# Optimization experiments

Measured on AMD Instinct MI355X. Metric: run time of the kernel, lower is better.

The kernel has to match this reference:

```python
import jax, jax.numpy as jnp
import numpy as np

NL = 4      # num_hidden_layers
NH = 12     # self-attn heads
CH = 4      # cross-attn heads (hardcoded in module)
S = 4       # speakers per dialog
EPS = 1e-5

def layernorm(x, g, b):
    m = x.mean(-1, keepdims=True)
    v = jnp.mean((x - m) ** 2, axis=-1, keepdims=True)
    return (x - m) * jax.lax.rsqrt(v + EPS) * g + b

def self_mha(x, in_w, in_b, out_w, out_b):
    # x: [B,T,L,H] self-attention over L (the per-turn token axis)
    B, T, L, H = x.shape
    dh = H // NH
    qkv = x @ in_w + in_b                       # [B,T,L,3H]
    q, k, v = jnp.split(qkv, 3, axis=-1)
    q = q.reshape(B, T, L, NH, dh); k = k.reshape(B, T, L, NH, dh); v = v.reshape(B, T, L, NH, dh)
    s = jnp.einsum('btqhd,btkhd->bthqk', q, k) / np.sqrt(dh).astype(x.dtype)
    a = jax.nn.softmax(s, axis=-1)
    o = jnp.einsum('bthqk,btkhd->btqhd', a, v).reshape(B, T, L, H)
    return o @ out_w + out_b

def forward(input_ids, attention_mask, speaker_ids, tok_emb, pos_emb, turn_emb,
            mha_in_w, mha_in_b, mha_out_w, mha_out_b,
            ffn_w1, ffn_b1, ffn_w2, ffn_b2,
            ln1_g, ln1_b, ln2_g, ln2_b,
            gate_w, gate_b, sn_g, sn_b,
            ca_in_w, ca_in_b, ca_out_w, ca_out_b):
    B, T, L = input_ids.shape
    H = tok_emb.shape[1]
    X = tok_emb[input_ids] + pos_emb[jnp.arange(L)][None, None] + turn_emb[jnp.arange(T)][None, :, None]
    mask = attention_mask[..., None].astype(X.dtype)            # [B,T,L,1]
    onehot = (speaker_ids[..., None] == jnp.arange(S)).astype(X.dtype)  # [B,T,S]
    counts = onehot.sum(1)                                      # [B,S]
    M = jnp.zeros((B, S, H), X.dtype)                           # speaker memory
    for l in range(NL):
        m_t = jnp.einsum('bts,bsh->bth', onehot, M)             # gather memory per turn
        h = (X + m_t[:, :, None, :]) * mask                     # mask applied by zeroing inputs (as in source)
        h = self_mha(h, mha_in_w[l], mha_in_b[l], mha_out_w[l], mha_out_b[l])
        h = layernorm(h + X, ln1_g[l], ln1_b[l])
        ffn = jax.nn.gelu(h @ ffn_w1[l] + ffn_b1[l], approximate=False) @ ffn_w2[l] + ffn_b2[l]
        h = layernorm(h + ffn, ln2_g[l], ln2_b[l])
        X = h
        tc = h.mean(2)                                          # token_context [B,T,H]
        # cross-attention: each turn's context queries its dialog's speaker memory
        wq, wk, wv = jnp.split(ca_in_w[l], 3, axis=-1)
        bq, bk, bv = jnp.split(ca_in_b[l], 3)
        dh = H // CH
        q = (tc @ wq + bq).reshape(B, T, CH, dh)
        k = (M @ wk + bk).reshape(B, S, CH, dh)
        v = (M @ wv + bv).reshape(B, S, CH, dh)
        s = jnp.einsum('bthd,bshd->bhts', q, k) / np.sqrt(dh).astype(X.dtype)
        a = jax.nn.softmax(s, axis=-1)
        cc = jnp.einsum('bhts,bshd->bthd', a, v).reshape(B, T, H) @ ca_out_w[l] + ca_out_b[l]
        fused = jnp.concatenate([tc, m_t, cc], axis=-1)         # [B,T,3H]
        upd = layernorm(fused @ gate_w[l] + gate_b[l] + m_t, sn_g[l], sn_b[l])
        # scatter: per-speaker mean over that speaker's turns; untouched speakers keep old memory
        sums = jnp.einsum('bts,bth->bsh', onehot, upd)
        mean = sums / jnp.maximum(counts, 1.0)[..., None]
        M = jnp.where((counts > 0)[..., None], mean, M)
    return X, M

def setup_inputs() -> dict:
    key = jax.random.key(0)
    ks = iter(jax.random.split(key, 32))
    B, T, L, H, F, V, P = 8, 64, 64, 768, 3072, 30522, 512
    n = lambda shape: jax.random.normal(next(ks), shape, jnp.float32) * 0.02
    return {
        'input_ids': jax.random.randint(next(ks), (B, T, L), 0, V, jnp.int32),
        'attention_mask': jax.random.randint(next(ks), (B, T, L), 0, 2, jnp.int32),
        'speaker_ids': jax.random.randint(next(ks), (B, T), 0, S, jnp.int32),
        'tok_emb': n((V, H)), 'pos_emb': n((P, H)), 'turn_emb': n((P, H)),
        'mha_in_w': n((NL, H, 3 * H)), 'mha_in_b': jnp.zeros((NL, 3 * H)),
        'mha_out_w': n((NL, H, H)), 'mha_out_b': jnp.zeros((NL, H)),
        'ffn_w1': n((NL, H, F)), 'ffn_b1': jnp.zeros((NL, F)),
        'ffn_w2': n((NL, F, H)), 'ffn_b2': jnp.zeros((NL, H)),
        'ln1_g': jnp.ones((NL, H)), 'ln1_b': jnp.zeros((NL, H)),
        'ln2_g': jnp.ones((NL, H)), 'ln2_b': jnp.zeros((NL, H)),
        'gate_w': n((NL, 3 * H, H)), 'gate_b': jnp.zeros((NL, H)),
        'sn_g': jnp.ones((NL, H)), 'sn_b': jnp.zeros((NL, H)),
        'ca_in_w': n((NL, H, 3 * H)), 'ca_in_b': jnp.zeros((NL, 3 * H)),
        'ca_out_w': n((NL, H, H)), 'ca_out_b': jnp.zeros((NL, H)),
    }

def reference(input_ids, attention_mask, speaker_ids, tok_emb, pos_emb, turn_emb,
              mha_in_w, mha_in_b, mha_out_w, mha_out_b,
              ffn_w1, ffn_b1, ffn_w2, ffn_b2,
              ln1_g, ln1_b, ln2_g, ln2_b,
              gate_w, gate_b, sn_g, sn_b,
              ca_in_w, ca_in_b, ca_out_w, ca_out_b):
    return forward(input_ids, attention_mask, speaker_ids, tok_emb, pos_emb, turn_emb,
                   mha_in_w, mha_in_b, mha_out_w, mha_out_b,
                   ffn_w1, ffn_b1, ffn_w2, ffn_b2,
                   ln1_g, ln1_b, ln2_g, ln2_b,
                   gate_w, gate_b, sn_g, sn_b,
                   ca_in_w, ca_in_b, ca_out_w, ca_out_b)
```

## Files before the change

kernel.cpp:

```cpp
#include <hip/hip_runtime.h>

using u16 = unsigned short;
using u32 = unsigned int;

#define DI __device__ __forceinline__

typedef __bf16 bf16x8 __attribute__((ext_vector_type(8)));
typedef float  f32x4  __attribute__((ext_vector_type(4)));

DI float b2f(u16 u){ u32 x = ((u32)u) << 16; float f; __builtin_memcpy(&f, &x, 4); return f; }
DI u16 f2b(float f){ __bf16 h = (__bf16)f; u16 r; __builtin_memcpy(&r, &h, 2); return r; }
DI float gelu_fast(float v){
    float u = v * (0.7978845608f + 0.0356774081f * v * v);
    float e = __expf(2.0f * u);
    float t = 1.0f - 2.0f / (e + 1.0f);
    return 0.5f * v * (1.0f + t);
}

#define GLOAD16(g, l) __builtin_amdgcn_global_load_lds( \
    (const __attribute__((address_space(1))) void*)(g), \
    (__attribute__((address_space(3))) void*)(l), 16, 0, 0)

template<int EPI>
__global__ __launch_bounds__(256)
void gemm_bt(const u16* __restrict__ A, const u16* __restrict__ Bt,
             const float* __restrict__ bias, void* __restrict__ Cout,
             int M, int N, int K)
{
    __shared__ u16 lA[128 * 32];
    __shared__ u16 lB[128 * 32];
    const int tid  = threadIdx.x;
    const int lane = tid & 63;
    const int w    = tid >> 6;
    const int wm   = w >> 1, wn = w & 1;

    const int nx = gridDim.x;
    const int nb = nx * gridDim.y;
    int bid = blockIdx.y * nx + blockIdx.x;
    if ((nb & 7) == 0) bid = ((bid & 7) * (nb >> 3)) + (bid >> 3);
    const int m0 = (bid / nx) * 128;
    const int n0 = (bid % nx) * 128;

    f32x4 acc[4][4] = {};

    const int srow = tid >> 2;
    const int scol = (tid & 3) * 8;
    int ar0 = m0 + srow;      if (ar0 > M - 1) ar0 = M - 1;
    int ar1 = m0 + 64 + srow; if (ar1 > M - 1) ar1 = M - 1;
    const u16* gA0 = A  + (size_t)ar0 * K + scol;
    const u16* gA1 = A  + (size_t)ar1 * K + scol;
    const u16* gB0 = Bt + (size_t)(n0 + srow) * K + scol;
    const u16* gB1 = Bt + (size_t)(n0 + 64 + srow) * K + scol;
    u16* dA = &lA[tid * 8];
    u16* dB = &lB[tid * 8];

    const int la = lane & 15, lg = lane >> 4;
    for (int k0 = 0; k0 < K; k0 += 32) {
        GLOAD16(gA0 + k0, dA);
        GLOAD16(gA1 + k0, dA + 2048);
        GLOAD16(gB0 + k0, dB);
        GLOAD16(gB1 + k0, dB + 2048);
        __syncthreads();
        bf16x8 af[4], bfr[4];
        #pragma unroll
        for (int i = 0; i < 4; i++)
            af[i] = *(const bf16x8*)&lA[(wm * 64 + i * 16 + la) * 32 + lg * 8];
        #pragma unroll
        for (int j = 0; j < 4; j++)
            bfr[j] = *(const bf16x8*)&lB[(wn * 64 + j * 16 + la) * 32 + lg * 8];
        #pragma unroll
        for (int i = 0; i < 4; i++)
            #pragma unroll
            for (int j = 0; j < 4; j++)
                acc[i][j] = __builtin_amdgcn_mfma_f32_16x16x32_bf16(af[i], bfr[j], acc[i][j], 0, 0, 0);
        __syncthreads();
    }

    #pragma unroll
    for (int i = 0; i < 4; i++) {
        const int rowb = m0 + wm * 64 + i * 16 + lg * 4;
        #pragma unroll
        for (int j = 0; j < 4; j++) {
            const int col = n0 + wn * 64 + j * 16 + la;
            const float bv = bias[col];
            #pragma unroll
            for (int r = 0; r < 4; r++) {
                const int rr = rowb + r;
                if (rr < M) {
                    float v = acc[i][j][r] + bv;
                    if constexpr (EPI == 1) v = gelu_fast(v);
                    if constexpr (EPI == 2) ((float*)Cout)[(size_t)rr * N + col] = v;
                    else                    ((u16*)Cout)[(size_t)rr * N + col] = f2b(v);
                }
            }
        }
    }
}

__global__ __launch_bounds__(256)
void transp_conv(const float* __restrict__ in, u16* __restrict__ out, int K, int N)
{
    __shared__ float tile[32][33];
    const int l = blockIdx.z;
    const float* inp = in + (size_t)l * K * N;
    u16* op = out + (size_t)l * K * N;
    const int kb = blockIdx.y * 32, nb = blockIdx.x * 32;
    const int tx = threadIdx.x, ty = threadIdx.y;
    #pragma unroll
    for (int i = 0; i < 32; i += 8)
        tile[ty + i][tx] = inp[(size_t)(kb + ty + i) * N + nb + tx];
    __syncthreads();
    #pragma unroll
    for (int i = 0; i < 32; i += 8)
        op[(size_t)(nb + ty + i) * K + kb + tx] = f2b(tile[tx][ty + i]);
}

__global__ __launch_bounds__(192)
void embed_k(const int* __restrict__ ids, const float* __restrict__ te,
             const float* __restrict__ pe, const float* __restrict__ ue,
             u16* __restrict__ X)
{
    const int tok = blockIdx.x;
    const int l = tok & 63;
    const int t = (tok >> 6) & 63;
    const int id = ids[tok];
    const int c = threadIdx.x * 4;
    float4 a = *(const float4*)&te[(size_t)id * 768 + c];
    float4 p = *(const float4*)&pe[(size_t)l * 768 + c];
    float4 u = *(const float4*)&ue[(size_t)t * 768 + c];
    ushort4 o;
    o.x = f2b(a.x + p.x + u.x); o.y = f2b(a.y + p.y + u.y);
    o.z = f2b(a.z + p.z + u.z); o.w = f2b(a.w + p.w + u.w);
    *(ushort4*)&X[(size_t)tok * 768 + c] = o;
}

__global__ __launch_bounds__(256)
void gather_mt(const float* __restrict__ M, const int* __restrict__ sid,
               float* __restrict__ mt)
{
    const int bt = blockIdx.x, b = bt >> 6, tid = threadIdx.x;
    const float* src = M + ((size_t)b * 4 + sid[bt]) * 768;
    float* dst = mt + (size_t)bt * 768;
    dst[tid] = src[tid]; dst[tid + 256] = src[tid + 256]; dst[tid + 512] = src[tid + 512];
}

__global__ __launch_bounds__(192)
void prep_ain(const u16* __restrict__ X, const float* __restrict__ mt,
              const int* __restrict__ mask, u16* __restrict__ Ain)
{
    const int tok = blockIdx.x, bt = tok >> 6;
    const float mk = (float)mask[tok];
    const int c = threadIdx.x * 4;
    ushort4 xv = *(const ushort4*)&X[(size_t)tok * 768 + c];
    float4 mv = *(const float4*)&mt[(size_t)bt * 768 + c];
    ushort4 o;
    o.x = f2b((b2f(xv.x) + mv.x) * mk); o.y = f2b((b2f(xv.y) + mv.y) * mk);
    o.z = f2b((b2f(xv.z) + mv.z) * mk); o.w = f2b((b2f(xv.w) + mv.w) * mk);
    *(ushort4*)&Ain[(size_t)tok * 768 + c] = o;
}

__global__ __launch_bounds__(256)
void attn_self(const u16* __restrict__ QKV, u16* __restrict__ O)
{
    __shared__ u16 lQ[64 * 64], lK[64 * 64], lVt[64 * 64], lP[64 * 64];
    __shared__ float lS[64 * 68];
    const int bt = blockIdx.x / 12, h = blockIdx.x % 12;
    const int tid = threadIdx.x, lane = tid & 63, w = tid >> 6;
    const size_t base = (size_t)bt * 64 * 2304;

    #pragma unroll
    for (int it = 0; it < 2; ++it) {
        const int slot = it * 256 + tid;
        const int l = slot >> 3, dc = (slot & 7) * 8;
        const u16* qp = QKV + base + (size_t)l * 2304 + h * 64 + dc;
        *(uint4*)&lQ[l * 64 + dc] = *(const uint4*)qp;
        *(uint4*)&lK[l * 64 + dc] = *(const uint4*)(qp + 768);
        uint4 vv = *(const uint4*)(qp + 1536);
        u16 tmp[8]; *(uint4*)tmp = vv;
        #pragma unroll
        for (int j = 0; j < 8; j++) lVt[(dc + j) * 64 + l] = tmp[j];
    }
    __syncthreads();

    const int la = lane & 15, lg = lane >> 4;
    {
        f32x4 sa[4] = {};
        #pragma unroll
        for (int kh = 0; kh < 64; kh += 32) {
            bf16x8 aq = *(const bf16x8*)&lQ[(w * 16 + la) * 64 + kh + lg * 8];
            #pragma unroll
            for (int fn = 0; fn < 4; ++fn) {
                bf16x8 bk = *(const bf16x8*)&lK[(fn * 16 + la) * 64 + kh + lg * 8];
                sa[fn] = __builtin_amdgcn_mfma_f32_16x16x32_bf16(aq, bk, sa[fn], 0, 0, 0);
            }
        }
        #pragma unroll
        for (int fn = 0; fn < 4; ++fn)
            #pragma unroll
            for (int r = 0; r < 4; ++r)
                lS[(w * 16 + lg * 4 + r) * 68 + fn * 16 + la] = sa[fn][r] * 0.125f;
    }
    __syncthreads();

    {
        const int row = tid >> 2, q4 = tid & 3;
        float e[16]; float mx = -1e30f;
        #pragma unroll
        for (int j = 0; j < 16; j++) { e[j] = lS[row * 68 + q4 * 16 + j]; mx = fmaxf(mx, e[j]); }
        mx = fmaxf(mx, __shfl_xor(mx, 1)); mx = fmaxf(mx, __shfl_xor(mx, 2));
        float sm = 0.f;
        #pragma unroll
        for (int j = 0; j < 16; j++) { e[j] = __expf(e[j] - mx); sm += e[j]; }
        sm += __shfl_xor(sm, 1); sm += __shfl_xor(sm, 2);
        const float inv = 1.0f / sm;
        #pragma unroll
        for (int j = 0; j < 16; j++) lP[row * 64 + q4 * 16 + j] = f2b(e[j] * inv);
    }
    __syncthreads();

    {
        f32x4 oa[4] = {};
        #pragma unroll
        for (int kh = 0; kh < 64; kh += 32) {
            bf16x8 ap = *(const bf16x8*)&lP[(w * 16 + la) * 64 + kh + lg * 8];
            #pragma unroll
            for (int fn = 0; fn < 4; ++fn) {
                bf16x8 bv = *(const bf16x8*)&lVt[(fn * 16 + la) * 64 + kh + lg * 8];
                oa[fn] = __builtin_amdgcn_mfma_f32_16x16x32_bf16(ap, bv, oa[fn], 0, 0, 0);
            }
        }
        const size_t ob = (size_t)bt * 64 * 768 + h * 64;
        #pragma unroll
        for (int fn = 0; fn < 4; ++fn)
            #pragma unroll
            for (int r = 0; r < 4; ++r)
                O[ob + (size_t)(w * 16 + lg * 4 + r) * 768 + fn * 16 + la] = f2b(oa[fn][r]);
    }
}

DI float wave_red(float v) {
    #pragma unroll
    for (int o = 32; o > 0; o >>= 1) v += __shfl_xor(v, o);
    return v;
}

__global__ __launch_bounds__(256)
void ln_res(const u16* __restrict__ a, const u16* __restrict__ b,
            const float* __restrict__ g, const float* __restrict__ be,
            u16* __restrict__ out)
{
    __shared__ float red[8];
    const int tid = threadIdx.x;
    const size_t off = (size_t)blockIdx.x * 768;
    float x0 = b2f(a[off + tid])       + b2f(b[off + tid]);
    float x1 = b2f(a[off + tid + 256]) + b2f(b[off + tid + 256]);
    float x2 = b2f(a[off + tid + 512]) + b2f(b[off + tid + 512]);
    float s = wave_red(x0 + x1 + x2);
    float ss = wave_red(x0 * x0 + x1 * x1 + x2 * x2);
    if ((tid & 63) == 0) { red[tid >> 6] = s; red[4 + (tid >> 6)] = ss; }
    __syncthreads();
    s = red[0] + red[1] + red[2] + red[3];
    ss = red[4] + red[5] + red[6] + red[7];
    const float mean = s * (1.f / 768.f);
    const float var = fmaxf(ss * (1.f / 768.f) - mean * mean, 0.f);
    const float inv = rsqrtf(var + 1e-5f);
    out[off + tid]       = f2b((x0 - mean) * inv * g[tid]       + be[tid]);
    out[off + tid + 256] = f2b((x1 - mean) * inv * g[tid + 256] + be[tid + 256]);
    out[off + tid + 512] = f2b((x2 - mean) * inv * g[tid + 512] + be[tid + 512]);
}

__global__ __launch_bounds__(256)
void ln_upd(const float* __restrict__ a, const float* __restrict__ b,
            const float* __restrict__ g, const float* __restrict__ be,
            float* __restrict__ out)
{
    __shared__ float red[8];
    const int tid = threadIdx.x;
    const size_t off = (size_t)blockIdx.x * 768;
    float x0 = a[off + tid]       + b[off + tid];
    float x1 = a[off + tid + 256] + b[off + tid + 256];
    float x2 = a[off + tid + 512] + b[off + tid + 512];
    float s = wave_red(x0 + x1 + x2);
    float ss = wave_red(x0 * x0 + x1 * x1 + x2 * x2);
    if ((tid & 63) == 0) { red[tid >> 6] = s; red[4 + (tid >> 6)] = ss; }
    __syncthreads();
    s = red[0] + red[1] + red[2] + red[3];
    ss = red[4] + red[5] + red[6] + red[7];
    const float mean = s * (1.f / 768.f);
    const float var = fmaxf(ss * (1.f / 768.f) - mean * mean, 0.f);
    const float inv = rsqrtf(var + 1e-5f);
    out[off + tid]       = (x0 - mean) * inv * g[tid]       + be[tid];
    out[off + tid + 256] = (x1 - mean) * inv * g[tid + 256] + be[tid + 256];
    out[off + tid + 512] = (x2 - mean) * inv * g[tid + 512] + be[tid + 512];
}

__global__ __launch_bounds__(256)
void tc_mean(const u16* __restrict__ X, u16* __restrict__ tcb)
{
    const int bt = blockIdx.x, tid = threadIdx.x;
    float s0 = 0, s1 = 0, s2 = 0;
    for (int l = 0; l < 64; ++l) {
        const u16* r = X + ((size_t)bt * 64 + l) * 768;
        s0 += b2f(r[tid]); s1 += b2f(r[tid + 256]); s2 += b2f(r[tid + 512]);
    }
    tcb[(size_t)bt * 768 + tid]       = f2b(s0 * (1.f / 64.f));
    tcb[(size_t)bt * 768 + tid + 256] = f2b(s1 * (1.f / 64.f));
    tcb[(size_t)bt * 768 + tid + 512] = f2b(s2 * (1.f / 64.f));
}

__global__ __launch_bounds__(256)
void conv_bf16(const float* __restrict__ in, u16* __restrict__ out, int n)
{
    const int i = blockIdx.x * 256 + threadIdx.x;
    if (i < n) out[i] = f2b(in[i]);
}

__global__ __launch_bounds__(256)
void zero_f32(float* __restrict__ buf, int n)
{
    const int i = blockIdx.x * 256 + threadIdx.x;
    if (i < n) buf[i] = 0.f;
}

__global__ __launch_bounds__(256)
void cross_attn(const u16* __restrict__ qc, const u16* __restrict__ kvc,
                u16* __restrict__ cca)
{
    __shared__ float q[768], kk[4][768], vv[4][768], sraw[16], aw[16];
    const int bt = blockIdx.x, b = bt >> 6, tid = threadIdx.x;
    #pragma unroll
    for (int i = 0; i < 3; i++) q[tid + i * 256] = b2f(qc[(size_t)bt * 768 + tid + i * 256]);
    #pragma unroll
    for (int i = 0; i < 12; i++) {
        const int idx = i * 256 + tid;
        const int s = idx / 768, d = idx % 768;
        kk[s][d] = b2f(kvc[(size_t)(b * 4 + s) * 1536 + d]);
        vv[s][d] = b2f(kvc[(size_t)(b * 4 + s) * 1536 + 768 + d]);
    }
    __syncthreads();
    if (tid < 16) {
        const int hh = tid >> 2, s = tid & 3;
        float acc = 0.f;
        for (int d = 0; d < 192; ++d) acc += q[hh * 192 + d] * kk[s][hh * 192 + d];
        sraw[tid] = acc * 0.07216878364870323f;
    }
    __syncthreads();
    if (tid < 4) {
        float m = -1e30f;
        for (int s = 0; s < 4; s++) m = fmaxf(m, sraw[tid * 4 + s]);
        float ee[4], sm = 0.f;
        for (int s = 0; s < 4; s++) { ee[s] = __expf(sraw[tid * 4 + s] - m); sm += ee[s]; }
        for (int s = 0; s < 4; s++) aw[tid * 4 + s] = ee[s] / sm;
    }
    __syncthreads();
    #pragma unroll
    for (int i = 0; i < 3; i++) {
        const int j = tid + i * 256;
        const int hh = j / 192;
        float v = aw[hh * 4 + 0] * vv[0][j] + aw[hh * 4 + 1] * vv[1][j]
                + aw[hh * 4 + 2] * vv[2][j] + aw[hh * 4 + 3] * vv[3][j];
        cca[(size_t)bt * 768 + j] = f2b(v);
    }
}

__global__ __launch_bounds__(256)
void concat_fused(const u16* __restrict__ tcb, const float* __restrict__ mt,
                  const u16* __restrict__ ccp, u16* __restrict__ Fu)
{
    const int bt = blockIdx.x, tid = threadIdx.x;
    u16* o = Fu + (size_t)bt * 2304;
    #pragma unroll
    for (int i = 0; i < 3; i++) {
        const int j = tid + i * 256;
        o[j]        = tcb[(size_t)bt * 768 + j];
        o[768 + j]  = f2b(mt[(size_t)bt * 768 + j]);
        o[1536 + j] = ccp[(size_t)bt * 768 + j];
    }
}

__global__ __launch_bounds__(256)
void scatter_mem(const float* __restrict__ upd, const int* __restrict__ sid,
                 const float* __restrict__ counts, float* __restrict__ M)
{
    const int bs = blockIdx.x, b = bs >> 2, s = bs & 3, tid = threadIdx.x;
    const float c = counts[bs];
    #pragma unroll
    for (int i = 0; i < 3; i++) {
        const int j = tid + i * 256;
        float acc = 0.f;
        for (int t = 0; t < 64; ++t)
            if (sid[b * 64 + t] == s) acc += upd[((size_t)b * 64 + t) * 768 + j];
        if (c > 0.f) M[(size_t)bs * 768 + j] = acc / fmaxf(c, 1.f);
    }
}

__global__ void calc_counts(const int* __restrict__ sid, float* __restrict__ counts)
{
    const int tid = threadIdx.x;
    if (tid < 32) {
        const int b = tid >> 2, s = tid & 3;
        float c = 0.f;
        for (int t = 0; t < 64; ++t) c += (sid[b * 64 + t] == s) ? 1.f : 0.f;
        counts[tid] = c;
    }
}

__global__ __launch_bounds__(256)
void final_out(const u16* __restrict__ Xb, const float* __restrict__ M,
               float* __restrict__ out)
{
    const size_t i = (size_t)blockIdx.x * 256 + threadIdx.x;
    const size_t NX = 25165824ull;
    if (i < NX) out[i] = b2f(Xb[i]);
    else if (i < NX + 24576ull) out[i] = M[i - NX];
}

extern "C" void kernel_launch(void* const* d_in, const int* in_sizes, int n_in,
                              void* d_out, int out_size, void* d_ws, size_t ws_size,
                              hipStream_t stream)
{
    const int*   input_ids = (const int*)d_in[0];
    const int*   attn_mask = (const int*)d_in[1];
    const int*   sid       = (const int*)d_in[2];
    const float* tok_emb   = (const float*)d_in[3];
    const float* pos_emb   = (const float*)d_in[4];
    const float* turn_emb  = (const float*)d_in[5];
    const float* mha_in_w  = (const float*)d_in[6];
    const float* mha_in_b  = (const float*)d_in[7];
    const float* mha_out_w = (const float*)d_in[8];
    const float* mha_out_b = (const float*)d_in[9];
    const float* ffn_w1    = (const float*)d_in[10];
    const float* ffn_b1    = (const float*)d_in[11];
    const float* ffn_w2    = (const float*)d_in[12];
    const float* ffn_b2    = (const float*)d_in[13];
    const float* ln1_g     = (const float*)d_in[14];
    const float* ln1_b     = (const float*)d_in[15];
    const float* ln2_g     = (const float*)d_in[16];
    const float* ln2_b     = (const float*)d_in[17];
    const float* gate_w    = (const float*)d_in[18];
    const float* gate_b    = (const float*)d_in[19];
    const float* sn_g      = (const float*)d_in[20];
    const float* sn_b      = (const float*)d_in[21];
    const float* ca_in_w   = (const float*)d_in[22];
    const float* ca_in_b   = (const float*)d_in[23];
    const float* ca_out_w  = (const float*)d_in[24];
    const float* ca_out_b  = (const float*)d_in[25];
    (void)in_sizes; (void)n_in; (void)out_size;

    const size_t MB = 1ull << 20;
    int NCA, NCF; bool allW;
    if      (ws_size >= 460 * MB) { NCA = 2; NCF = 1; allW = true;  }
    else if (ws_size >= 255 * MB) { NCA = 2; NCF = 2; allW = false; }
    else                          { NCA = 4; NCF = 4; allW = false; }
    const int MRA = 32768 / NCA;
    const int MRF = 32768 / NCF;
    const size_t wl = allW ? 4 : 1;

    char* p = (char*)d_ws;
    auto alloc = [&](size_t n) { void* r = p; p += (n + 255) & ~(size_t)255; return r; };
    u16*   Xb    = (u16*)alloc(50331648);
    u16*   Hb    = (u16*)alloc(50331648);
    u16*   WqkvT = (u16*)alloc(wl * 3538944);
    u16*   WoT   = (u16*)alloc(wl * 1179648);
    u16*   W1T   = (u16*)alloc(wl * 4718592);
    u16*   W2T   = (u16*)alloc(wl * 4718592);
    u16*   WgT   = (u16*)alloc(wl * 3538944);
    u16*   WcaT  = (u16*)alloc(wl * 3538944);
    u16*   WcoT  = (u16*)alloc(wl * 1179648);
    float* mt    = (float*)alloc(1572864);
    u16*   tcb   = (u16*)alloc(786432);
    u16*   Mb    = (u16*)alloc(49152);
    u16*   qc    = (u16*)alloc(786432);
    u16*   kvc   = (u16*)alloc(98304);
    u16*   cca   = (u16*)alloc(786432);
    u16*   ccp   = (u16*)alloc(786432);
    u16*   Fu    = (u16*)alloc(2359296);
    float* gout  = (float*)alloc(1572864);
    float* upd   = (float*)alloc(1572864);
    float* cnts  = (float*)alloc(256);
    float* M     = (float*)alloc(98304);

    u16 *A, *QKVb, *Gb;
    if (NCF == 1) {
        A    = (u16*)alloc(50331648);
        Gb   = (u16*)alloc(201326592);
        QKVb = (u16*)d_out;
    } else if (NCF == 2) {
        A    = (u16*)alloc(50331648);
        QKVb = (u16*)alloc((size_t)MRA * 2304 * 2);
        Gb   = (u16*)d_out;
    } else {
        Gb   = (u16*)alloc((size_t)MRF * 3072 * 2);
        A    = (u16*)d_out;
        QKVb = (u16*)d_out + 25165824;
    }
    u16* Obuf = Gb;

    zero_f32<<<96, 256, 0, stream>>>(M, 24576);
    calc_counts<<<1, 64, 0, stream>>>(sid, cnts);
    embed_k<<<32768, 192, 0, stream>>>(input_ids, tok_emb, pos_emb, turn_emb, Xb);

    if (allW) {
        transp_conv<<<dim3(72, 24, 4), dim3(32, 8), 0, stream>>>(mha_in_w,  WqkvT, 768, 2304);
        transp_conv<<<dim3(24, 24, 4), dim3(32, 8), 0, stream>>>(mha_out_w, WoT,   768, 768);
        transp_conv<<<dim3(96, 24, 4), dim3(32, 8), 0, stream>>>(ffn_w1,    W1T,   768, 3072);
        transp_conv<<<dim3(24, 96, 4), dim3(32, 8), 0, stream>>>(ffn_w2,    W2T,  3072, 768);
        transp_conv<<<dim3(24, 72, 4), dim3(32, 8), 0, stream>>>(gate_w,    WgT,  2304, 768);
        transp_conv<<<dim3(72, 24, 4), dim3(32, 8), 0, stream>>>(ca_in_w,   WcaT,  768, 2304);
        transp_conv<<<dim3(24, 24, 4), dim3(32, 8), 0, stream>>>(ca_out_w,  WcoT,  768, 768);
    }

    for (int l = 0; l < 4; ++l) {
        if (!allW) {
            transp_conv<<<dim3(72, 24), dim3(32, 8), 0, stream>>>(mha_in_w  + (size_t)l * 768 * 2304, WqkvT, 768, 2304);
            transp_conv<<<dim3(24, 24), dim3(32, 8), 0, stream>>>(mha_out_w + (size_t)l * 768 * 768,  WoT,   768, 768);
            transp_conv<<<dim3(96, 24), dim3(32, 8), 0, stream>>>(ffn_w1    + (size_t)l * 768 * 3072, W1T,   768, 3072);
            transp_conv<<<dim3(24, 96), dim3(32, 8), 0, stream>>>(ffn_w2    + (size_t)l * 3072 * 768, W2T,  3072, 768);
            transp_conv<<<dim3(24, 72), dim3(32, 8), 0, stream>>>(gate_w    + (size_t)l * 2304 * 768, WgT,  2304, 768);
            transp_conv<<<dim3(72, 24), dim3(32, 8), 0, stream>>>(ca_in_w   + (size_t)l * 768 * 2304, WcaT,  768, 2304);
            transp_conv<<<dim3(24, 24), dim3(32, 8), 0, stream>>>(ca_out_w  + (size_t)l * 768 * 768,  WcoT,  768, 768);
        }
        const u16* Wqkv_l = WqkvT + (size_t)(allW ? l : 0) * 2304 * 768;
        const u16* Wo_l   = WoT   + (size_t)(allW ? l : 0) * 768 * 768;
        const u16* W1_l   = W1T   + (size_t)(allW ? l : 0) * 768 * 3072;
        const u16* W2_l   = W2T   + (size_t)(allW ? l : 0) * 3072 * 768;
        const u16* Wg_l   = WgT   + (size_t)(allW ? l : 0) * 2304 * 768;
        const u16* Wca_l  = WcaT  + (size_t)(allW ? l : 0) * 768 * 2304;
        const u16* Wco_l  = WcoT  + (size_t)(allW ? l : 0) * 768 * 768;

        gather_mt<<<512, 256, 0, stream>>>(M, sid, mt);
        prep_ain<<<32768, 192, 0, stream>>>(Xb, mt, attn_mask, A);

        for (int c = 0; c < NCA; ++c) {
            u16* Ac = A + (size_t)c * MRA * 768;
            gemm_bt<0><<<dim3(18, MRA / 128), 256, 0, stream>>>(Ac, Wqkv_l, mha_in_b + l * 2304, QKVb, MRA, 2304, 768);
            attn_self<<<(MRA / 64) * 12, 256, 0, stream>>>(QKVb, Obuf);
            gemm_bt<0><<<dim3(6, MRA / 128), 256, 0, stream>>>(Obuf, Wo_l, mha_out_b + l * 768, Ac, MRA, 768, 768);
        }
        ln_res<<<32768, 256, 0, stream>>>(A, Xb, ln1_g + l * 768, ln1_b + l * 768, Hb);

        for (int c = 0; c < NCF; ++c) {
            u16* Hc = Hb + (size_t)c * MRF * 768;
            u16* Ac = A  + (size_t)c * MRF * 768;
            gemm_bt<1><<<dim3(24, MRF / 128), 256, 0, stream>>>(Hc, W1_l, ffn_b1 + l * 3072, Gb, MRF, 3072, 768);
            gemm_bt<0><<<dim3(6, MRF / 128), 256, 0, stream>>>(Gb, W2_l, ffn_b2 + l * 768, Ac, MRF, 768, 3072);
        }
        ln_res<<<32768, 256, 0, stream>>>(A, Hb, ln2_g + l * 768, ln2_b + l * 768, Xb);

        tc_mean<<<512, 256, 0, stream>>>(Xb, tcb);
        conv_bf16<<<96, 256, 0, stream>>>(M, Mb, 24576);
        gemm_bt<0><<<dim3(6, 4), 256, 0, stream>>>(tcb, WcaT + (size_t)(allW ? l : 0) * 768 * 2304, ca_in_b + l * 2304, qc, 512, 768, 768);
        gemm_bt<0><<<dim3(12, 1), 256, 0, stream>>>(Mb, Wca_l + 768 * 768, ca_in_b + l * 2304 + 768, kvc, 32, 1536, 768);
        cross_attn<<<512, 256, 0, stream>>>(qc, kvc, cca);
        gemm_bt<0><<<dim3(6, 4), 256, 0, stream>>>(cca, Wco_l, ca_out_b + l * 768, ccp, 512, 768, 768);
        concat_fused<<<512, 256, 0, stream>>>(tcb, mt, ccp, Fu);
        gemm_bt<2><<<dim3(6, 4), 256, 0, stream>>>(Fu, Wg_l, gate_b + l * 768, gout, 512, 768, 2304);
        ln_upd<<<512, 256, 0, stream>>>(gout, mt, sn_g + l * 768, sn_b + l * 768, upd);
        scatter_mem<<<32, 256, 0, stream>>>(upd, sid, cnts, M);
    }

    final_out<<<98400, 256, 0, stream>>>(Xb, M, (float*)d_out);
}
```

Before: 4.352 ms.

## Double-buffer GEMM LDS tiles, swizzle LDS layouts in GEMM and attention

The GEMM kernel now keeps two LDS stages, so global-to-LDS loads for the next K tile are issued while MFMAs run on the current one, with one barrier per iteration instead of two. The GEMM and self-attention LDS layouts use XOR swizzles to reduce bank conflicts on fragment reads. The cross-attention query projection now reads the Wca_l pointer instead of WcaT. This doubles GEMM LDS use, which can lower occupancy, and the weight-pointer change may alter which weights are used.

```diff
diff --git a/kernel.cpp b/kernel.cpp
--- a/kernel.cpp
+++ b/kernel.cpp
@@ -21,14 +21,20 @@
     (const __attribute__((address_space(1))) void*)(g), \
     (__attribute__((address_space(3))) void*)(l), 16, 0, 0)
 
+#define HARD_BARRIER() do { \
+    asm volatile("s_waitcnt vmcnt(0)" ::: "memory"); \
+    __builtin_amdgcn_s_barrier(); \
+    asm volatile("" ::: "memory"); \
+} while (0)
+
 template<int EPI>
 __global__ __launch_bounds__(256)
 void gemm_bt(const u16* __restrict__ A, const u16* __restrict__ Bt,
              const float* __restrict__ bias, void* __restrict__ Cout,
              int M, int N, int K)
 {
-    __shared__ u16 lA[128 * 32];
-    __shared__ u16 lB[128 * 32];
+    __shared__ u16 lA[2][128 * 32];
+    __shared__ u16 lB[2][128 * 32];
     const int tid  = threadIdx.x;
     const int lane = tid & 63;
     const int w    = tid >> 6;
@@ -44,36 +50,49 @@
     f32x4 acc[4][4] = {};
 
     const int srow = tid >> 2;
-    const int scol = (tid & 3) * 8;
+    const int scol = (((tid & 3) ^ ((tid >> 3) & 3)) * 8);
     int ar0 = m0 + srow;      if (ar0 > M - 1) ar0 = M - 1;
     int ar1 = m0 + 64 + srow; if (ar1 > M - 1) ar1 = M - 1;
     const u16* gA0 = A  + (size_t)ar0 * K + scol;
     const u16* gA1 = A  + (size_t)ar1 * K + scol;
     const u16* gB0 = Bt + (size_t)(n0 + srow) * K + scol;
     const u16* gB1 = Bt + (size_t)(n0 + 64 + srow) * K + scol;
-    u16* dA = &lA[tid * 8];
-    u16* dB = &lB[tid * 8];
 
     const int la = lane & 15, lg = lane >> 4;
-    for (int k0 = 0; k0 < K; k0 += 32) {
-        GLOAD16(gA0 + k0, dA);
-        GLOAD16(gA1 + k0, dA + 2048);
-        GLOAD16(gB0 + k0, dB);
-        GLOAD16(gB1 + k0, dB + 2048);
-        __syncthreads();
+    const int cp = (lg ^ ((la >> 1) & 3)) * 8;
+
+    const int nt = K >> 5;
+
+    GLOAD16(gA0, &lA[0][tid * 8]);
+    GLOAD16(gA1, &lA[0][tid * 8 + 2048]);
+    GLOAD16(gB0, &lB[0][tid * 8]);
+    GLOAD16(gB1, &lB[0][tid * 8 + 2048]);
+    HARD_BARRIER();
+
+    int cur = 0;
+    for (int t = 0; t < nt; ++t) {
+        if (t + 1 < nt) {
+            const int k0 = (t + 1) << 5;
+            const int b = cur ^ 1;
+            GLOAD16(gA0 + k0, &lA[b][tid * 8]);
+            GLOAD16(gA1 + k0, &lA[b][tid * 8 + 2048]);
+            GLOAD16(gB0 + k0, &lB[b][tid * 8]);
+            GLOAD16(gB1 + k0, &lB[b][tid * 8 + 2048]);
+        }
         bf16x8 af[4], bfr[4];
         #pragma unroll
         for (int i = 0; i < 4; i++)
-            af[i] = *(const bf16x8*)&lA[(wm * 64 + i * 16 + la) * 32 + lg * 8];
+            af[i] = *(const bf16x8*)&lA[cur][(wm * 64 + i * 16 + la) * 32 + cp];
         #pragma unroll
         for (int j = 0; j < 4; j++)
-            bfr[j] = *(const bf16x8*)&lB[(wn * 64 + j * 16 + la) * 32 + lg * 8];
+            bfr[j] = *(const bf16x8*)&lB[cur][(wn * 64 + j * 16 + la) * 32 + cp];
         #pragma unroll
         for (int i = 0; i < 4; i++)
             #pragma unroll
             for (int j = 0; j < 4; j++)
                 acc[i][j] = __builtin_amdgcn_mfma_f32_16x16x32_bf16(af[i], bfr[j], acc[i][j], 0, 0, 0);
-        __syncthreads();
+        HARD_BARRIER();
+        cur ^= 1;
     }
 
     #pragma unroll
@@ -159,6 +178,8 @@
     *(ushort4*)&Ain[(size_t)tok * 768 + c] = o;
 }
 
+DI int swz(int row, int col) { return row * 64 + (((col >> 3) ^ (row & 7)) << 3) + (col & 7); }
+
 __global__ __launch_bounds__(256)
 void attn_self(const u16* __restrict__ QKV, u16* __restrict__ O)
 {
@@ -173,12 +194,12 @@
         const int slot = it * 256 + tid;
         const int l = slot >> 3, dc = (slot & 7) * 8;
         const u16* qp = QKV + base + (size_t)l * 2304 + h * 64 + dc;
-        *(uint4*)&lQ[l * 64 + dc] = *(const uint4*)qp;
-        *(uint4*)&lK[l * 64 + dc] = *(const uint4*)(qp + 768);
+        *(uint4*)&lQ[swz(l, dc)] = *(const uint4*)qp;
+        *(uint4*)&lK[swz(l, dc)] = *(const uint4*)(qp + 768);
         uint4 vv = *(const uint4*)(qp + 1536);
         u16 tmp[8]; *(uint4*)tmp = vv;
         #pragma unroll
-        for (int j = 0; j < 8; j++) lVt[(dc + j) * 64 + l] = tmp[j];
+        for (int j = 0; j < 8; j++) lVt[swz(dc + j, l)] = tmp[j];
     }
     __syncthreads();
 
@@ -187,10 +208,10 @@
         f32x4 sa[4] = {};
         #pragma unroll
         for (int kh = 0; kh < 64; kh += 32) {
-            bf16x8 aq = *(const bf16x8*)&lQ[(w * 16 + la) * 64 + kh + lg * 8];
+            bf16x8 aq = *(const bf16x8*)&lQ[swz(w * 16 + la, kh + lg * 8)];
             #pragma unroll
             for (int fn = 0; fn < 4; ++fn) {
-                bf16x8 bk = *(const bf16x8*)&lK[(fn * 16 + la) * 64 + kh + lg * 8];
+                bf16x8 bk = *(const bf16x8*)&lK[swz(fn * 16 + la, kh + lg * 8)];
                 sa[fn] = __builtin_amdgcn_mfma_f32_16x16x32_bf16(aq, bk, sa[fn], 0, 0, 0);
             }
         }
@@ -214,7 +235,7 @@
         sm += __shfl_xor(sm, 1); sm += __shfl_xor(sm, 2);
         const float inv = 1.0f / sm;
         #pragma unroll
-        for (int j = 0; j < 16; j++) lP[row * 64 + q4 * 16 + j] = f2b(e[j] * inv);
+        for (int j = 0; j < 16; j++) lP[swz(row, q4 * 16 + j)] = f2b(e[j] * inv);
     }
     __syncthreads();
 
@@ -222,10 +243,10 @@
         f32x4 oa[4] = {};
         #pragma unroll
         for (int kh = 0; kh < 64; kh += 32) {
-            bf16x8 ap = *(const bf16x8*)&lP[(w * 16 + la) * 64 + kh + lg * 8];
+            bf16x8 ap = *(const bf16x8*)&lP[swz(w * 16 + la, kh + lg * 8)];
             #pragma unroll
             for (int fn = 0; fn < 4; ++fn) {
-                bf16x8 bv = *(const bf16x8*)&lVt[(fn * 16 + la) * 64 + kh + lg * 8];
+                bf16x8 bv = *(const bf16x8*)&lVt[swz(fn * 16 + la, kh + lg * 8)];
                 oa[fn] = __builtin_amdgcn_mfma_f32_16x16x32_bf16(ap, bv, oa[fn], 0, 0, 0);
             }
         }
@@ -549,7 +570,7 @@
 
         tc_mean<<<512, 256, 0, stream>>>(Xb, tcb);
         conv_bf16<<<96, 256, 0, stream>>>(M, Mb, 24576);
-        gemm_bt<0><<<dim3(6, 4), 256, 0, stream>>>(tcb, WcaT + (size_t)(allW ? l : 0) * 768 * 2304, ca_in_b + l * 2304, qc, 512, 768, 768);
+        gemm_bt<0><<<dim3(6, 4), 256, 0, stream>>>(tcb, Wca_l, ca_in_b + l * 2304, qc, 512, 768, 768);
         gemm_bt<0><<<dim3(12, 1), 256, 0, stream>>>(Mb, Wca_l + 768 * 768, ca_in_b + l * 2304 + 768, kvc, 32, 1536, 768);
         cross_attn<<<512, 256, 0, stream>>>(qc, kvc, cca);
         gemm_bt<0><<<dim3(6, 4), 256, 0, stream>>>(cca, Wco_l, ca_out_b + l * 768, ccp, 512, 768, 768);
```

Result: faster. 4.238 ms (-2.6%).
